# Kernel optimization log

Hardware: AMD Instinct MI355X
Metric: run time of the kernel (lower is better)

The kernel has to match this reference:

```python
import jax, jax.numpy as jnp
import numpy as np

B = 64        # number of graphs in the batch
NPG = 1024    # nodes per graph (uniform batch_num_nodes)
N = B * NPG   # total nodes = 65536
D = 512       # input feature dim
DEG = 32      # average degree
K = 0.5       # keep-percent
DROP = NPG - int(np.ceil(K * NPG))  # number of lowest-score nodes zeroed per graph


def setup_inputs() -> dict:
    key = jax.random.key(0)
    k1, k2, k3, k4 = jax.random.split(key, 4)
    features = jax.random.normal(k1, (N, D), dtype=jnp.float32)
    # edges constrained inside each graph's node block (batched DGL graph is block-diagonal)
    offsets = (jnp.arange(B, dtype=jnp.int64) * NPG)[:, None]
    src = (jax.random.randint(k2, (B, NPG * DEG), 0, NPG, dtype=jnp.int64) + offsets).reshape(-1)
    dst = (jax.random.randint(k3, (B, NPG * DEG), 0, NPG, dtype=jnp.int64) + offsets).reshape(-1)
    # GraphConv(input_dim=D, out=1) parameters (glorot-ish scale)
    weight = jax.random.normal(k4, (D, 1), dtype=jnp.float32) * (1.0 / np.sqrt(D))
    bias = jnp.zeros((1,), dtype=jnp.float32)
    return {"features": features, "src": src, "dst": dst, "weight": weight, "bias": bias}


def reference(features, src, dst, weight, bias):
    # --- GraphConv(D -> 1, norm=True, bias=True, activation=relu) ---
    # old-DGL norm=True: symmetric normalization with in-degrees, norm=deg^-0.5 (0 for isolated)
    deg = jnp.zeros((N,), features.dtype).at[dst].add(1.0)
    norm = jnp.where(deg > 0, deg ** -0.5, 0.0)[:, None]          # [N,1]
    # in_feats > out_feats: project first, then aggregate scalars
    h = (features @ weight) * norm                                # [N,1]
    agg = jnp.zeros_like(h).at[dst].add(h[src])                   # sum over in-edges
    w = jax.nn.relu(agg * norm + bias)                            # [N,1] scores
    # --- per-graph top-k masking: zero the DROP smallest scores in each graph ---
    wb = w.reshape(B, NPG)
    ranks = jnp.argsort(jnp.argsort(wb, axis=1), axis=1)          # rank 0 = smallest
    wb = jnp.where(ranks < DROP, jnp.zeros((), wb.dtype), wb)
    # --- elementwise gating of features by (masked) scores ---
    return features * wb.reshape(N, 1)
```

## Files before the change

kernel.cpp:

```cpp
#include <hip/hip_runtime.h>

#define NTOT 65536
#define DIM  512
#define BGR  64
#define NPG  1024
#define DROPN 512
#define SLICES 8
#define DEG_BLOCKS 64
#define MV_BLOCKS 2048

typedef float vf4 __attribute__((ext_vector_type(4)));
typedef unsigned long long u64;

__global__ __launch_bounds__(256) void k1_matvec_deg(
        const float* __restrict__ X, const float* __restrict__ W,
        const int* __restrict__ dst,
        float* __restrict__ p, float* __restrict__ norm, int epg) {
    __shared__ int dl[NPG];
    if (blockIdx.x < DEG_BLOCKS) {
        const int g = blockIdx.x;
        const int nbase = g * NPG;
        for (int i = threadIdx.x; i < NPG; i += 256) dl[i] = 0;
        __syncthreads();
        const int4* d4 = (const int4*)(dst + (size_t)g * epg);
        const int n4 = epg >> 2;
        for (int i = threadIdx.x; i < n4; i += 256) {
            int4 d = d4[i];
            atomicAdd(&dl[d.x - nbase], 1);
            atomicAdd(&dl[d.y - nbase], 1);
            atomicAdd(&dl[d.z - nbase], 1);
            atomicAdd(&dl[d.w - nbase], 1);
        }
        __syncthreads();
        for (int i = threadIdx.x; i < NPG; i += 256) {
            int d = dl[i];
            norm[nbase + i] = d > 0 ? rsqrtf((float)d) : 0.f;
        }
    } else {
        const int lane = threadIdx.x & 63;
        const int wid  = ((blockIdx.x - DEG_BLOCKS) * 256 + threadIdx.x) >> 6;
        const int nw   = (MV_BLOCKS * 256) >> 6;
        const vf4* wr = (const vf4*)W;
        const vf4 w0 = wr[lane], w1 = wr[lane + 64];
        for (int row = wid; row < NTOT; row += 2 * nw) {
            const int row2 = row + nw;
            const vf4* xr0 = (const vf4*)(X + (size_t)row  * DIM);
            const vf4* xr1 = (const vf4*)(X + (size_t)row2 * DIM);
            vf4 a0 = xr0[lane], a1 = xr0[lane + 64];
            vf4 b0 = xr1[lane], b1 = xr1[lane + 64];
            vf4 m0 = a0 * w0 + a1 * w1;
            vf4 m1 = b0 * w0 + b1 * w1;
            float s0 = m0[0] + m0[1] + m0[2] + m0[3];
            float s1 = m1[0] + m1[1] + m1[2] + m1[3];
            #pragma unroll
            for (int off = 32; off > 0; off >>= 1) {
                s0 += __shfl_down(s0, off, 64);
                s1 += __shfl_down(s1, off, 64);
            }
            if (lane == 0) { p[row] = s0; p[row2] = s1; }
        }
    }
}

__global__ __launch_bounds__(256) void k2_agg(
        const int* __restrict__ src, const int* __restrict__ dst,
        const float* __restrict__ p, const float* __restrict__ norm,
        float* __restrict__ agg_part, int epg) {
    __shared__ float hl[NPG];
    __shared__ float al[NPG];
    const int b = blockIdx.x;
    const int g = b & (BGR - 1);
    const int slice = b >> 6;
    const int nbase = g * NPG;
    const int eps = epg / SLICES;
    for (int i = threadIdx.x; i < NPG; i += 256) {
        hl[i] = p[nbase + i] * norm[nbase + i];
        al[i] = 0.f;
    }
    __syncthreads();
    const int4* s4 = (const int4*)(src + (size_t)g * epg + (size_t)slice * eps);
    const int4* d4 = (const int4*)(dst + (size_t)g * epg + (size_t)slice * eps);
    const int n4 = eps >> 2;
    for (int i = threadIdx.x; i < n4; i += 256) {
        int4 s = s4[i];
        int4 d = d4[i];
        atomicAdd(&al[d.x - nbase], hl[s.x - nbase]);
        atomicAdd(&al[d.y - nbase], hl[s.y - nbase]);
        atomicAdd(&al[d.z - nbase], hl[s.z - nbase]);
        atomicAdd(&al[d.w - nbase], hl[s.w - nbase]);
    }
    __syncthreads();
    float* op = agg_part + (size_t)slice * NTOT + nbase;
    for (int i = threadIdx.x; i < NPG; i += 256) op[i] = al[i];
}

__global__ __launch_bounds__(1024) void k3_topk(
        const float* __restrict__ agg_part, const float* __restrict__ norm,
        const float* __restrict__ bias, float* __restrict__ gate) {
    __shared__ unsigned int hist[256];
    __shared__ unsigned int selbin, selkp;
    __shared__ unsigned int wsum[16];
    const int g = blockIdx.x;
    const int t = threadIdx.x;
    const int lane = t & 63;
    const int wid  = t >> 6;
    const int nbase = g * NPG;
    float a = 0.f;
    #pragma unroll
    for (int s = 0; s < SLICES; s++) a += agg_part[(size_t)s * NTOT + nbase + t];
    float w = a * norm[nbase + t] + bias[0];
    w = w > 0.f ? w : 0.f;
    const unsigned int v = __float_as_uint(w);
    bool act = true;
    unsigned int kp = DROPN;
    unsigned int T = 0;
    #pragma unroll
    for (int shift = 24; shift >= 0; shift -= 8) {
        if (t < 256) hist[t] = 0;
        __syncthreads();
        const unsigned int byte = (v >> shift) & 255u;
        if (act) atomicAdd(&hist[byte], 1u);
        __syncthreads();
        if (t < 64) {
            unsigned int h0 = hist[t*4], h1 = hist[t*4+1], h2 = hist[t*4+2], h3 = hist[t*4+3];
            unsigned int lsum = h0 + h1 + h2 + h3;
            unsigned int x = lsum;
            #pragma unroll
            for (int off = 1; off < 64; off <<= 1) {
                unsigned int y = (unsigned int)__shfl_up((int)x, off, 64);
                if (lane >= off) x += y;
            }
            unsigned int excl = x - lsum;
            hist[t*4]   = excl + h0;
            hist[t*4+1] = excl + h0 + h1;
            hist[t*4+2] = excl + h0 + h1 + h2;
            hist[t*4+3] = excl + h0 + h1 + h2 + h3;
        }
        __syncthreads();
        if (t < 256) {
            unsigned int lo = (t == 0) ? 0u : hist[t-1];
            unsigned int hi = hist[t];
            if (lo <= kp && kp < hi) { selbin = (unsigned int)t; selkp = kp - lo; }
        }
        __syncthreads();
        const unsigned int b = selbin;
        kp = selkp;
        act = act && (byte == b);
        T |= b << shift;
    }
    u64 bal = __ballot(act);
    if (lane == 0) wsum[wid] = (unsigned int)__popcll(bal);
    __syncthreads();
    unsigned int wpre = 0;
    for (int i = 0; i < wid; i++) wpre += wsum[i];
    unsigned int eqrank = wpre + (unsigned int)__popcll(bal & ((1ull << lane) - 1ull));
    bool keep = act ? (eqrank >= kp) : (v > T);
    gate[nbase + t] = keep ? w : 0.f;
}

__global__ __launch_bounds__(256) void k4_gate(
        const float* __restrict__ X, const float* __restrict__ gate,
        float* __restrict__ out) {
    const int lane = threadIdx.x & 63;
    const int nw   = (gridDim.x * blockDim.x) >> 6;
    const int wid  = (blockIdx.x * blockDim.x + threadIdx.x) >> 6;
    for (int row = wid; row < NTOT; row += nw) {
        float g = gate[row];
        vf4* o = (vf4*)(out + (size_t)row * DIM);
        if (g == 0.f) {
            vf4 z = (vf4){0.f, 0.f, 0.f, 0.f};
            __builtin_nontemporal_store(z, &o[lane]);
            __builtin_nontemporal_store(z, &o[lane + 64]);
        } else {
            const vf4* xr = (const vf4*)(X + (size_t)row * DIM);
            vf4 a = xr[lane] * g;
            vf4 c = xr[lane + 64] * g;
            __builtin_nontemporal_store(a, &o[lane]);
            __builtin_nontemporal_store(c, &o[lane + 64]);
        }
    }
}

extern "C" void kernel_launch(void* const* d_in, const int* in_sizes, int n_in,
                              void* d_out, int out_size, void* d_ws, size_t ws_size,
                              hipStream_t stream) {
    const float* X    = (const float*)d_in[0];
    const int*   src  = (const int*)d_in[1];
    const int*   dst  = (const int*)d_in[2];
    const float* W    = (const float*)d_in[3];
    const float* bias = (const float*)d_in[4];
    float* out = (float*)d_out;
    int E   = in_sizes[1];
    int epg = E / BGR;

    float* ws       = (float*)d_ws;
    float* p        = ws;
    float* norm     = ws + 1 * NTOT;
    float* gate     = ws + 2 * NTOT;
    float* agg_part = ws + 3 * NTOT;

    k1_matvec_deg<<<DEG_BLOCKS + MV_BLOCKS, 256, 0, stream>>>(X, W, dst, p, norm, epg);
    k2_agg<<<BGR * SLICES, 256, 0, stream>>>(src, dst, p, norm, agg_part, epg);
    k3_topk<<<BGR, 1024, 0, stream>>>(agg_part, norm, bias, gate);
    k4_gate<<<2048, 256, 0, stream>>>(X, gate, out);
}
```

Baseline: 276.9 us.

## Fuse aggregation and top-k into one kernel via last-block ticket

The separate top-k kernel is merged into the aggregation kernel. Each slice block now atomically adds its partial sums into a shared global agg buffer, and a per-graph ticket counter picks the last-arriving block to run the radix-select top-k with 256 threads handling 4 nodes each. The agg buffer and tickets are zeroed in the degree blocks of the first kernel. This removes one kernel launch and the 8-slice partial buffer round trip, at the cost of global float atomics and a serialized tail done by one block per graph.

```diff
diff --git a/kernel.cpp b/kernel.cpp
--- a/kernel.cpp
+++ b/kernel.cpp
@@ -15,12 +15,15 @@
 __global__ __launch_bounds__(256) void k1_matvec_deg(
         const float* __restrict__ X, const float* __restrict__ W,
         const int* __restrict__ dst,
-        float* __restrict__ p, float* __restrict__ norm, int epg) {
+        float* __restrict__ p, float* __restrict__ norm,
+        float* __restrict__ agg, int* __restrict__ ticket, int epg) {
     __shared__ int dl[NPG];
     if (blockIdx.x < DEG_BLOCKS) {
         const int g = blockIdx.x;
         const int nbase = g * NPG;
         for (int i = threadIdx.x; i < NPG; i += 256) dl[i] = 0;
+        ((vf4*)(agg + nbase))[threadIdx.x] = (vf4){0.f, 0.f, 0.f, 0.f};
+        if (threadIdx.x == 0) ticket[g] = 0;
         __syncthreads();
         const int4* d4 = (const int4*)(dst + (size_t)g * epg);
         const int n4 = epg >> 2;
@@ -62,26 +65,35 @@
     }
 }
 
-__global__ __launch_bounds__(256) void k2_agg(
+__global__ __launch_bounds__(256) void k2_agg_topk(
         const int* __restrict__ src, const int* __restrict__ dst,
         const float* __restrict__ p, const float* __restrict__ norm,
-        float* __restrict__ agg_part, int epg) {
+        const float* __restrict__ bias,
+        float* __restrict__ agg, int* __restrict__ ticket,
+        float* __restrict__ gate, int epg) {
     __shared__ float hl[NPG];
     __shared__ float al[NPG];
+    __shared__ unsigned int hist[256];
+    __shared__ unsigned int selbin, selkp;
+    __shared__ unsigned int wsum[4];
+    __shared__ int lastFlag;
     const int b = blockIdx.x;
     const int g = b & (BGR - 1);
     const int slice = b >> 6;
     const int nbase = g * NPG;
     const int eps = epg / SLICES;
-    for (int i = threadIdx.x; i < NPG; i += 256) {
-        hl[i] = p[nbase + i] * norm[nbase + i];
-        al[i] = 0.f;
+    const int t = threadIdx.x;
+    {
+        const vf4* pv = (const vf4*)(p + nbase);
+        const vf4* nv = (const vf4*)(norm + nbase);
+        ((vf4*)hl)[t] = pv[t] * nv[t];
+        ((vf4*)al)[t] = (vf4){0.f, 0.f, 0.f, 0.f};
     }
     __syncthreads();
     const int4* s4 = (const int4*)(src + (size_t)g * epg + (size_t)slice * eps);
     const int4* d4 = (const int4*)(dst + (size_t)g * epg + (size_t)slice * eps);
     const int n4 = eps >> 2;
-    for (int i = threadIdx.x; i < n4; i += 256) {
+    for (int i = t; i < n4; i += 256) {
         int4 s = s4[i];
         int4 d = d4[i];
         atomicAdd(&al[d.x - nbase], hl[s.x - nbase]);
@@ -90,36 +102,43 @@
         atomicAdd(&al[d.w - nbase], hl[s.w - nbase]);
     }
     __syncthreads();
-    float* op = agg_part + (size_t)slice * NTOT + nbase;
-    for (int i = threadIdx.x; i < NPG; i += 256) op[i] = al[i];
-}
-
-__global__ __launch_bounds__(1024) void k3_topk(
-        const float* __restrict__ agg_part, const float* __restrict__ norm,
-        const float* __restrict__ bias, float* __restrict__ gate) {
-    __shared__ unsigned int hist[256];
-    __shared__ unsigned int selbin, selkp;
-    __shared__ unsigned int wsum[16];
-    const int g = blockIdx.x;
-    const int t = threadIdx.x;
-    const int lane = t & 63;
-    const int wid  = t >> 6;
-    const int nbase = g * NPG;
-    float a = 0.f;
-    #pragma unroll
-    for (int s = 0; s < SLICES; s++) a += agg_part[(size_t)s * NTOT + nbase + t];
-    float w = a * norm[nbase + t] + bias[0];
-    w = w > 0.f ? w : 0.f;
-    const unsigned int v = __float_as_uint(w);
-    bool act = true;
+    #pragma unroll
+    for (int c = 0; c < 4; c++) {
+        int i = t + 256 * c;
+        atomicAdd(&agg[nbase + i], al[i]);
+    }
+    __threadfence();
+    if (t == 0) lastFlag = (atomicAdd(&ticket[g], 1) == SLICES - 1);
+    __syncthreads();
+    if (!lastFlag) return;
+    __threadfence();
+    const float bb = bias[0];
+    float w[4];
+    unsigned int v[4];
+    bool act[4];
+    const vf4* nv = (const vf4*)(norm + nbase);
+    vf4 nrm4 = nv[t];
+    #pragma unroll
+    for (int c = 0; c < 4; c++) {
+        int i = 4 * t + c;
+        float a = atomicAdd(&agg[nbase + i], 0.f);
+        float ww = a * nrm4[c] + bb;
+        ww = ww > 0.f ? ww : 0.f;
+        w[c] = ww;
+        v[c] = __float_as_uint(ww);
+        act[c] = true;
+    }
     unsigned int kp = DROPN;
     unsigned int T = 0;
+    const int lane = t & 63;
+    const int wv   = t >> 6;
     #pragma unroll
     for (int shift = 24; shift >= 0; shift -= 8) {
-        if (t < 256) hist[t] = 0;
-        __syncthreads();
-        const unsigned int byte = (v >> shift) & 255u;
-        if (act) atomicAdd(&hist[byte], 1u);
+        hist[t] = 0;
+        __syncthreads();
+        #pragma unroll
+        for (int c = 0; c < 4; c++)
+            if (act[c]) atomicAdd(&hist[(v[c] >> shift) & 255u], 1u);
         __syncthreads();
         if (t < 64) {
             unsigned int h0 = hist[t*4], h1 = hist[t*4+1], h2 = hist[t*4+2], h3 = hist[t*4+3];
@@ -137,28 +156,44 @@
             hist[t*4+3] = excl + h0 + h1 + h2 + h3;
         }
         __syncthreads();
-        if (t < 256) {
+        {
             unsigned int lo = (t == 0) ? 0u : hist[t-1];
             unsigned int hi = hist[t];
             if (lo <= kp && kp < hi) { selbin = (unsigned int)t; selkp = kp - lo; }
         }
         __syncthreads();
-        const unsigned int b = selbin;
+        const unsigned int sb = selbin;
         kp = selkp;
-        act = act && (byte == b);
-        T |= b << shift;
-    }
-    u64 bal = __ballot(act);
-    if (lane == 0) wsum[wid] = (unsigned int)__popcll(bal);
-    __syncthreads();
-    unsigned int wpre = 0;
-    for (int i = 0; i < wid; i++) wpre += wsum[i];
-    unsigned int eqrank = wpre + (unsigned int)__popcll(bal & ((1ull << lane) - 1ull));
-    bool keep = act ? (eqrank >= kp) : (v > T);
-    gate[nbase + t] = keep ? w : 0.f;
-}
-
-__global__ __launch_bounds__(256) void k4_gate(
+        #pragma unroll
+        for (int c = 0; c < 4; c++)
+            act[c] = act[c] && (((v[c] >> shift) & 255u) == sb);
+        T |= sb << shift;
+    }
+    int cnt = 0;
+    int pre[4];
+    #pragma unroll
+    for (int c = 0; c < 4; c++) { pre[c] = cnt; cnt += act[c] ? 1 : 0; }
+    int x = cnt;
+    #pragma unroll
+    for (int off = 1; off < 64; off <<= 1) {
+        int y = __shfl_up(x, off, 64);
+        if (lane >= off) x += y;
+    }
+    if (lane == 63) wsum[wv] = (unsigned int)x;
+    __syncthreads();
+    int base = 0;
+    for (int i = 0; i < wv; i++) base += (int)wsum[i];
+    const int excl = base + x - cnt;
+    vf4 gout;
+    #pragma unroll
+    for (int c = 0; c < 4; c++) {
+        bool keep = act[c] ? ((unsigned int)(excl + pre[c]) >= kp) : (v[c] > T);
+        gout[c] = keep ? w[c] : 0.f;
+    }
+    ((vf4*)(gate + nbase))[t] = gout;
+}
+
+__global__ __launch_bounds__(256) void k3_gate(
         const float* __restrict__ X, const float* __restrict__ gate,
         float* __restrict__ out) {
     const int lane = threadIdx.x & 63;
@@ -193,14 +228,14 @@
     int E   = in_sizes[1];
     int epg = E / BGR;
 
-    float* ws       = (float*)d_ws;
-    float* p        = ws;
-    float* norm     = ws + 1 * NTOT;
-    float* gate     = ws + 2 * NTOT;
-    float* agg_part = ws + 3 * NTOT;
-
-    k1_matvec_deg<<<DEG_BLOCKS + MV_BLOCKS, 256, 0, stream>>>(X, W, dst, p, norm, epg);
-    k2_agg<<<BGR * SLICES, 256, 0, stream>>>(src, dst, p, norm, agg_part, epg);
-    k3_topk<<<BGR, 1024, 0, stream>>>(agg_part, norm, bias, gate);
-    k4_gate<<<2048, 256, 0, stream>>>(X, gate, out);
-}
+    float* ws     = (float*)d_ws;
+    float* p      = ws;
+    float* norm   = ws + 1 * NTOT;
+    float* gate   = ws + 2 * NTOT;
+    float* agg    = ws + 3 * NTOT;
+    int*   ticket = (int*)(ws + 4 * NTOT);
+
+    k1_matvec_deg<<<DEG_BLOCKS + MV_BLOCKS, 256, 0, stream>>>(X, W, dst, p, norm, agg, ticket, epg);
+    k2_agg_topk<<<BGR * SLICES, 256, 0, stream>>>(src, dst, p, norm, bias, agg, ticket, gate, epg);
+    k3_gate<<<2048, 256, 0, stream>>>(X, gate, out);
+}
```

Measured after the change: 306.9 us. +10.8%, slower.
